# Performance work log

Hardware: AMD Instinct MI355X
Metric: run time of the kernel (lower is better)

Reference implementation:

```python
import jax, jax.numpy as jnp
import numpy as np

IMG_SIZE = 224
PATCH_SIZE = 16
CONTEXT_LEN = 316
LATENT_DIM = 1024
NUM_HEADS = 16
NUM_PATCHES = (IMG_SIZE // PATCH_SIZE) ** 2  # 196
SEQ_LEN = NUM_PATCHES + CONTEXT_LEN          # 512
BATCH = 8


def prefix_lm_mask(num_img_patches, total):
    # lower-triangular causal mask, but the image-patch block is fully bidirectional
    m = np.tril(np.ones((total, total), dtype=np.float32))
    m[:num_img_patches, :num_img_patches] = 1.0
    return jnp.asarray(m)  # [S, S], 1 = attend, 0 = masked


def setup_inputs() -> dict:
    key = jax.random.key(0)
    k_x, k_q, k_k, k_v, k_o, k_b = jax.random.split(key, 6)
    d = LATENT_DIM
    scale = 1.0 / np.sqrt(d)
    return {
        "x": jax.random.normal(k_x, (BATCH, SEQ_LEN, d), dtype=jnp.float32),
        "w_q": jax.random.normal(k_q, (d, d), dtype=jnp.float32) * scale,
        "w_k": jax.random.normal(k_k, (d, d), dtype=jnp.float32) * scale,
        "w_v": jax.random.normal(k_v, (d, d), dtype=jnp.float32) * scale,
        "w_o": jax.random.normal(k_o, (d, d), dtype=jnp.float32) * scale,
        "b_o": jax.random.normal(k_b, (d,), dtype=jnp.float32) * 0.01,
    }


def reference(x, w_q, w_k, w_v, w_o, b_o):
    B, S, D = x.shape
    H = NUM_HEADS
    hd = D // H
    # projections (nn.Linear: y = x @ W^T)
    q = (x @ w_q.T).reshape(B, S, H, hd).transpose(0, 2, 1, 3)  # [B,H,S,hd]
    k = (x @ w_k.T).reshape(B, S, H, hd).transpose(0, 2, 1, 3)
    v = (x @ w_v.T).reshape(B, S, H, hd).transpose(0, 2, 1, 3)
    scores = jnp.einsum("bhqd,bhkd->bhqk", q, k) / jnp.sqrt(jnp.float32(hd))
    mask = prefix_lm_mask(NUM_PATCHES, S)  # [S,S]
    scores = jnp.where(mask == 0, jnp.float32(-jnp.inf), scores)
    attn = jax.nn.softmax(scores, axis=-1)
    ctx = jnp.einsum("bhqk,bhkd->bhqd", attn, v)
    ctx = ctx.transpose(0, 2, 1, 3).reshape(B, S, D)
    return ctx @ w_o.T + b_o
```

## Files before the change

### kernel.cpp

```cpp
#include <hip/hip_runtime.h>
#include <stdint.h>
#include <math.h>

#define NB_B 8
#define NB_S 512
#define NB_D 1024
#define NB_H 16
#define NB_HD 64
#define NP 196
#define MTOT 4096

#define OFF_XB 0
#define OFF_WQ 4194304
#define OFF_WK 5242880
#define OFF_WV 6291456
#define OFF_WO 7340032
#define OFF_Q  8388608
#define OFF_K  12582912
#define OFF_VT 16777216
#define OFF_CT 20971520

typedef __attribute__((ext_vector_type(8))) short bf16x8;
typedef __attribute__((ext_vector_type(4))) float f32x4;
typedef __attribute__((ext_vector_type(4))) short s16x4;

__device__ __forceinline__ short f2bf(float f) {
  union { float f; uint32_t u; } c; c.f = f;
  uint32_t r = (c.u + 0x7fffu + ((c.u >> 16) & 1u)) >> 16;
  return (short)r;
}

__device__ __forceinline__ uint32_t pack2bf(float lo, float hi) {
  uint32_t ulo = __float_as_uint(lo) + 0x8000u;
  uint32_t uhi = __float_as_uint(hi) + 0x8000u;
  return __builtin_amdgcn_perm(uhi, ulo, 0x07060302u);
}

__device__ __forceinline__ void async16(void* lds, const void* g) {
  __builtin_amdgcn_global_load_lds(
      (const __attribute__((address_space(1))) void*)g,
      (__attribute__((address_space(3))) void*)lds, 16, 0, 0);
}

__global__ __launch_bounds__(256) void cvt5(const float* __restrict__ x,
                                            const float* __restrict__ wq,
                                            const float* __restrict__ wk,
                                            const float* __restrict__ wv,
                                            const float* __restrict__ wo,
                                            short* __restrict__ ws) {
  int b = blockIdx.x, t = threadIdx.x;
  const float* src; short* dst; float scale;
  if (b < 4096) { src = x + b * 1024; dst = ws + OFF_XB + b * 1024; scale = 1.0f; }
  else {
    int wb = b - 4096, wi = wb >> 10, r = wb & 1023;
    switch (wi) {
      case 0:  src = wq + r * 1024; dst = ws + OFF_WQ + r * 1024; scale = 0.125f; break;
      case 1:  src = wk + r * 1024; dst = ws + OFF_WK + r * 1024; scale = 1.0f;   break;
      case 2:  src = wv + r * 1024; dst = ws + OFF_WV + r * 1024; scale = 1.0f;   break;
      default: src = wo + r * 1024; dst = ws + OFF_WO + r * 1024; scale = 1.0f;   break;
    }
  }
  int i = t << 2;
  float4 v = *(const float4*)(src + i);
  s16x4 o;
  o[0] = f2bf(v.x * scale); o[1] = f2bf(v.y * scale);
  o[2] = f2bf(v.z * scale); o[3] = f2bf(v.w * scale);
  *(s16x4*)(dst + i) = o;
}

__global__ __launch_bounds__(256, 2) void gemm_qkv(short* __restrict__ ws) {
  __shared__ __align__(16) short As[4096];
  __shared__ __align__(16) short Bs[4096];
  int bx = blockIdx.x;
  int wsel = bx >> 8;
  int tile = bx & 255;
  int mt = tile >> 3, nt = tile & 7;
  int m0 = mt << 7, n0 = nt << 7;
  const short* A  = ws + OFF_XB;
  const short* Bw = ws + (wsel == 0 ? OFF_WQ : (wsel == 1 ? OFF_WK : OFF_WV));
  int t = threadIdx.x, lane = t & 63, wvi = t >> 6;
  int c = lane & 15, quad = lane >> 4;
  int wm = wvi >> 1, wn = wvi & 1;
  f32x4 acc[4][4] = {};

  for (int kk = 0; kk < 1024; kk += 32) {
#pragma unroll
    for (int i = 0; i < 2; ++i) {
      int ch = wvi * 2 + i;
      const short* ga = A  + (m0 + ch * 16 + c) * 1024 + kk + (quad << 3);
      async16(&As[ch << 9], ga);
      const short* gb = Bw + (n0 + ch * 16 + c) * 1024 + kk + (quad << 3);
      async16(&Bs[ch << 9], gb);
    }
    __syncthreads();
    bf16x8 af[4], bfr[4];
#pragma unroll
    for (int i = 0; i < 4; ++i) af[i]  = *(const bf16x8*)&As[((wm * 4 + i) * 64 + lane) * 8];
#pragma unroll
    for (int j = 0; j < 4; ++j) bfr[j] = *(const bf16x8*)&Bs[((wn * 4 + j) * 64 + lane) * 8];
#pragma unroll
    for (int i = 0; i < 4; ++i)
#pragma unroll
      for (int j = 0; j < 4; ++j)
        acc[i][j] = __builtin_amdgcn_mfma_f32_16x16x32_bf16(af[i], bfr[j], acc[i][j], 0, 0, 0);
    __syncthreads();
  }

  short* outp = ws + (wsel == 0 ? OFF_Q : (wsel == 1 ? OFF_K : OFF_VT));
#pragma unroll
  for (int i = 0; i < 4; ++i) {
#pragma unroll
    for (int j = 0; j < 4; ++j) {
      int n = n0 + wn * 64 + j * 16 + c;
      int h = n >> 6, d = n & 63;
      int mq = m0 + wm * 64 + i * 16 + quad * 4;
      int bb = mq >> 9, s = mq & 511;
      if (wsel < 2) {
#pragma unroll
        for (int r = 0; r < 4; ++r)
          outp[((bb * 16 + h) * 512 + (s + r)) * 64 + d] = f2bf(acc[i][j][r]);
      } else {
        s16x4 o;
#pragma unroll
        for (int r = 0; r < 4; ++r) o[r] = f2bf(acc[i][j][r]);
        *(s16x4*)&outp[((bb * 16 + h) * 64 + d) * 512 + s] = o;
      }
    }
  }
}

__global__ __launch_bounds__(256, 2) void attn(short* __restrict__ ws) {
  __shared__ __align__(16) short Kb[4096];
  __shared__ __align__(16) short Vb[4096];
  int bi = blockIdx.x;
  int bh = bi >> 2, qcr = bi & 3;
  int qc = (qcr + bh + 2 * (bh >> 6)) & 3;
  int t = threadIdx.x, lane = t & 63, wvi = t >> 6;
  int c = lane & 15, quad = lane >> 4;
  const short* Qh  = ws + OFF_Q  + bh * (512 * 64);
  const short* Kh  = ws + OFF_K  + bh * (512 * 64);
  const short* Vth = ws + OFF_VT + bh * (64 * 512);
  short* ctx = ws + OFF_CT;
  int b = bh >> 4, h = bh & 15;

  int qt0 = qc * 128 + wvi * 32;
  int qt1 = qt0 + 16;
  int kn0 = (qt0 + 16 > NP) ? (qt0 + 16) : NP;
  int kn1 = (qt1 + 16 > NP) ? (qt1 + 16) : NP;
  int knb = (qc * 128 + 128 > NP) ? (qc * 128 + 128) : NP;
  int NCH = (knb + 63) >> 6;

  bf16x8 q00 = *(const bf16x8*)(Qh + (qt0 + c) * 64 + (quad << 3));
  bf16x8 q01 = *(const bf16x8*)(Qh + (qt0 + c) * 64 + 32 + (quad << 3));
  bf16x8 q10 = *(const bf16x8*)(Qh + (qt1 + c) * 64 + (quad << 3));
  bf16x8 q11 = *(const bf16x8*)(Qh + (qt1 + c) * 64 + 32 + (quad << 3));

  f32x4 acc0[4] = {}, acc1[4] = {};
  float l0 = 0.0f, l1 = 0.0f;
  int L0 = c + ((quad & 1) << 5);
  bool hilo = quad >= 2;

  for (int ch = 0; ch < NCH; ++ch) {
    int k0 = ch << 6;
    {
      const short* gk = Kh + (k0 + wvi * 16 + c) * 64 + (quad << 3);
      async16(&Kb[(wvi * 2 + 0) << 9], gk);
      async16(&Kb[(wvi * 2 + 1) << 9], gk + 32);
      const short* gv = Vth + (wvi * 16 + c) * 512 + k0 + (quad << 3);
      async16(&Vb[(wvi * 2 + 0) << 9], gv);
      async16(&Vb[(wvi * 2 + 1) << 9], gv + 32);
    }
    __syncthreads();

    bf16x8 ak[4][2], av[4][2];
#pragma unroll
    for (int mb = 0; mb < 4; ++mb)
#pragma unroll
      for (int f = 0; f < 2; ++f) {
        ak[mb][f] = *(const bf16x8*)&Kb[((mb * 2 + f) << 9) + lane * 8];
        av[mb][f] = *(const bf16x8*)&Vb[((mb * 2 + f) << 9) + lane * 8];
      }

#pragma unroll
    for (int s = 0; s < 2; ++s) {
      int qt = s ? qt1 : qt0;
      int kn = s ? kn1 : kn0;
      if (k0 >= kn) continue;
      bf16x8 bq0 = s ? q10 : q00;
      bf16x8 bq1 = s ? q11 : q01;
      f32x4* acc = s ? acc1 : acc0;

      float p[4][4];
#pragma unroll
      for (int mb = 0; mb < 4; ++mb) {
        f32x4 st = {};
        st = __builtin_amdgcn_mfma_f32_16x16x32_bf16(ak[mb][0], bq0, st, 0, 0, 0);
        st = __builtin_amdgcn_mfma_f32_16x16x32_bf16(ak[mb][1], bq1, st, 0, 0, 0);
#pragma unroll
        for (int r = 0; r < 4; ++r) p[mb][r] = __expf(st[r]);
      }

      if ((k0 + 64 > NP) && (k0 + 64 > qt + 1)) {
        int row = qt + c;
#pragma unroll
        for (int mb = 0; mb < 4; ++mb)
#pragma unroll
          for (int r = 0; r < 4; ++r) {
            int key = k0 + mb * 16 + (quad << 2) + r;
            bool v = (row < NP) ? (key < NP) : (key <= row);
            p[mb][r] = v ? p[mb][r] : 0.0f;
          }
      }
      float ls = 0.0f;
#pragma unroll
      for (int mb = 0; mb < 4; ++mb)
#pragma unroll
        for (int r = 0; r < 4; ++r) ls += p[mb][r];
      if (s) l1 += ls; else l0 += ls;

#pragma unroll
      for (int hh = 0; hh < 2; ++hh) {
        float* pa = p[2 * hh];
        float* pb = p[2 * hh + 1];
        uint32_t e0 = pack2bf(pa[0], pa[1]);
        uint32_t e1 = pack2bf(pa[2], pa[3]);
        uint32_t e2 = pack2bf(pb[0], pb[1]);
        uint32_t e3 = pack2bf(pb[2], pb[3]);
        uint32_t a0 = (uint32_t)__shfl((int)e0, L0);
        uint32_t b0 = (uint32_t)__shfl((int)e1, L0);
        uint32_t a1 = (uint32_t)__shfl((int)e0, L0 + 16);
        uint32_t b1 = (uint32_t)__shfl((int)e1, L0 + 16);
        uint32_t c0 = (uint32_t)__shfl((int)e2, L0);
        uint32_t d0 = (uint32_t)__shfl((int)e3, L0);
        uint32_t c1 = (uint32_t)__shfl((int)e2, L0 + 16);
        uint32_t d1 = (uint32_t)__shfl((int)e3, L0 + 16);
        union { uint32_t u[4]; bf16x8 v; } bp;
        bp.u[0] = hilo ? c0 : a0;
        bp.u[1] = hilo ? d0 : b0;
        bp.u[2] = hilo ? c1 : a1;
        bp.u[3] = hilo ? d1 : b1;
#pragma unroll
        for (int db = 0; db < 4; ++db)
          acc[db] = __builtin_amdgcn_mfma_f32_16x16x32_bf16(av[db][hh], bp.v, acc[db], 0, 0, 0);
      }
    }
    __syncthreads();
  }

#pragma unroll
  for (int s = 0; s < 2; ++s) {
    float l = s ? l1 : l0;
    f32x4* acc = s ? acc1 : acc0;
    int qt = s ? qt1 : qt0;
    l += __shfl_xor(l, 16);
    l += __shfl_xor(l, 32);
    float inv = 1.0f / l;
    size_t rowbase = ((size_t)(b * 512 + qt + c)) * 1024 + h * 64 + (quad << 2);
#pragma unroll
    for (int db = 0; db < 4; ++db) {
      s16x4 o;
#pragma unroll
      for (int r = 0; r < 4; ++r) o[r] = f2bf(acc[db][r] * inv);
      *(s16x4*)&ctx[rowbase + db * 16] = o;
    }
  }
}

__global__ __launch_bounds__(256, 2) void gemm_out(const short* __restrict__ ws,
                                                   const float* __restrict__ bias,
                                                   float* __restrict__ out) {
  __shared__ __align__(16) short As[4096];
  __shared__ __align__(16) short Bs[4096];
  int tile = blockIdx.x;
  int mt = tile >> 3, nt = tile & 7;
  int m0 = mt << 7, n0 = nt << 7;
  const short* A  = ws + OFF_CT;
  const short* Bw = ws + OFF_WO;
  int t = threadIdx.x, lane = t & 63, wvi = t >> 6;
  int c = lane & 15, quad = lane >> 4;
  int wm = wvi >> 1, wn = wvi & 1;
  f32x4 acc[4][4] = {};

  for (int kk = 0; kk < 1024; kk += 32) {
#pragma unroll
    for (int i = 0; i < 2; ++i) {
      int ch = wvi * 2 + i;
      async16(&As[ch << 9], A  + (m0 + ch * 16 + c) * 1024 + kk + (quad << 3));
      async16(&Bs[ch << 9], Bw + (n0 + ch * 16 + c) * 1024 + kk + (quad << 3));
    }
    __syncthreads();
    bf16x8 af[4], bfr[4];
#pragma unroll
    for (int i = 0; i < 4; ++i) af[i]  = *(const bf16x8*)&As[((wm * 4 + i) * 64 + lane) * 8];
#pragma unroll
    for (int j = 0; j < 4; ++j) bfr[j] = *(const bf16x8*)&Bs[((wn * 4 + j) * 64 + lane) * 8];
#pragma unroll
    for (int i = 0; i < 4; ++i)
#pragma unroll
      for (int j = 0; j < 4; ++j)
        acc[i][j] = __builtin_amdgcn_mfma_f32_16x16x32_bf16(af[i], bfr[j], acc[i][j], 0, 0, 0);
    __syncthreads();
  }

#pragma unroll
  for (int j = 0; j < 4; ++j) {
    int n = n0 + wn * 64 + j * 16 + c;
    float bj = bias[n];
#pragma unroll
    for (int i = 0; i < 4; ++i) {
      int mq = m0 + wm * 64 + i * 16 + quad * 4;
#pragma unroll
      for (int r = 0; r < 4; ++r)
        out[(size_t)(mq + r) * 1024 + n] = acc[i][j][r] + bj;
    }
  }
}

extern "C" void kernel_launch(void* const* d_in, const int* in_sizes, int n_in,
                              void* d_out, int out_size, void* d_ws, size_t ws_size,
                              hipStream_t stream) {
  (void)in_sizes; (void)n_in; (void)out_size; (void)ws_size;
  const float* x  = (const float*)d_in[0];
  const float* wq = (const float*)d_in[1];
  const float* wk = (const float*)d_in[2];
  const float* wv = (const float*)d_in[3];
  const float* wo = (const float*)d_in[4];
  const float* bo = (const float*)d_in[5];
  short* ws = (short*)d_ws;
  float* out = (float*)d_out;

  cvt5<<<8192, 256, 0, stream>>>(x, wq, wk, wv, wo, ws);
  gemm_qkv<<<768, 256, 0, stream>>>(ws);
  attn<<<512, 256, 0, stream>>>(ws);
  gemm_out<<<256, 256, 0, stream>>>(ws, bo, out);
}
```

Before: 188.6 us.

## Fuse Q, K, V projections into one GEMM tile sharing the activation tile

The QKV projection kernel now gives each block a 64-row slice of x and computes 128 columns of all three of Q, K and V together. Each loaded A tile is reused across the three weight matrices instead of being reloaded by three separate blocks. This cuts global and LDS traffic for the activations and shrinks the grid from 768 to 512 blocks. In exchange, LDS use rises to about 28 KB per block and each wave holds 24 accumulator tiles, which raises register pressure and may lower occupancy.

Result: slower. 195.1 us (+3.4%).

```diff
diff --git a/kernel.cpp b/kernel.cpp
--- a/kernel.cpp
+++ b/kernel.cpp
@@ -69,61 +69,67 @@
 }
 
 __global__ __launch_bounds__(256, 2) void gemm_qkv(short* __restrict__ ws) {
-  __shared__ __align__(16) short As[4096];
-  __shared__ __align__(16) short Bs[4096];
+  __shared__ __align__(16) short Ls[14336];
   int bx = blockIdx.x;
-  int wsel = bx >> 8;
-  int tile = bx & 255;
-  int mt = tile >> 3, nt = tile & 7;
-  int m0 = mt << 7, n0 = nt << 7;
-  const short* A  = ws + OFF_XB;
-  const short* Bw = ws + (wsel == 0 ? OFF_WQ : (wsel == 1 ? OFF_WK : OFF_WV));
+  int mt = bx >> 3, nt = bx & 7;
+  int m0 = mt << 6, n0 = nt << 7;
+  const short* A = ws + OFF_XB;
   int t = threadIdx.x, lane = t & 63, wvi = t >> 6;
   int c = lane & 15, quad = lane >> 4;
-  int wm = wvi >> 1, wn = wvi & 1;
-  f32x4 acc[4][4] = {};
+  f32x4 acc[3][4][2] = {};
 
   for (int kk = 0; kk < 1024; kk += 32) {
 #pragma unroll
-    for (int i = 0; i < 2; ++i) {
-      int ch = wvi * 2 + i;
-      const short* ga = A  + (m0 + ch * 16 + c) * 1024 + kk + (quad << 3);
-      async16(&As[ch << 9], ga);
-      const short* gb = Bw + (n0 + ch * 16 + c) * 1024 + kk + (quad << 3);
-      async16(&Bs[ch << 9], gb);
-    }
-    __syncthreads();
-    bf16x8 af[4], bfr[4];
-#pragma unroll
-    for (int i = 0; i < 4; ++i) af[i]  = *(const bf16x8*)&As[((wm * 4 + i) * 64 + lane) * 8];
-#pragma unroll
-    for (int j = 0; j < 4; ++j) bfr[j] = *(const bf16x8*)&Bs[((wn * 4 + j) * 64 + lane) * 8];
-#pragma unroll
-    for (int i = 0; i < 4; ++i)
-#pragma unroll
-      for (int j = 0; j < 4; ++j)
-        acc[i][j] = __builtin_amdgcn_mfma_f32_16x16x32_bf16(af[i], bfr[j], acc[i][j], 0, 0, 0);
-    __syncthreads();
-  }
-
-  short* outp = ws + (wsel == 0 ? OFF_Q : (wsel == 1 ? OFF_K : OFF_VT));
-#pragma unroll
-  for (int i = 0; i < 4; ++i) {
-#pragma unroll
-    for (int j = 0; j < 4; ++j) {
-      int n = n0 + wn * 64 + j * 16 + c;
+    for (int i = 0; i < 7; ++i) {
+      int ch = wvi * 7 + i;
+      const short* src;
+      if (ch < 4) {
+        src = A + (m0 + ch * 16 + c) * 1024 + kk + (quad << 3);
+      } else {
+        int cw = (ch - 4) >> 3, cb = (ch - 4) & 7;
+        src = ws + OFF_WQ + cw * 1048576 + (n0 + cb * 16 + c) * 1024 + kk + (quad << 3);
+      }
+      async16(&Ls[ch << 9], src);
+    }
+    __syncthreads();
+
+    bf16x8 af[4];
+#pragma unroll
+    for (int mb = 0; mb < 4; ++mb) af[mb] = *(const bf16x8*)&Ls[(mb << 9) + lane * 8];
+#pragma unroll
+    for (int w = 0; w < 3; ++w) {
+#pragma unroll
+      for (int nb = 0; nb < 2; ++nb) {
+        bf16x8 bf = *(const bf16x8*)&Ls[((4 + w * 8 + wvi * 2 + nb) << 9) + lane * 8];
+#pragma unroll
+        for (int mb = 0; mb < 4; ++mb)
+          acc[w][mb][nb] = __builtin_amdgcn_mfma_f32_16x16x32_bf16(af[mb], bf, acc[w][mb][nb], 0, 0, 0);
+      }
+    }
+    __syncthreads();
+  }
+
+#pragma unroll
+  for (int w = 0; w < 3; ++w) {
+#pragma unroll
+    for (int nb = 0; nb < 2; ++nb) {
+      int n = n0 + wvi * 32 + nb * 16 + c;
       int h = n >> 6, d = n & 63;
-      int mq = m0 + wm * 64 + i * 16 + quad * 4;
-      int bb = mq >> 9, s = mq & 511;
-      if (wsel < 2) {
-#pragma unroll
-        for (int r = 0; r < 4; ++r)
-          outp[((bb * 16 + h) * 512 + (s + r)) * 64 + d] = f2bf(acc[i][j][r]);
-      } else {
-        s16x4 o;
-#pragma unroll
-        for (int r = 0; r < 4; ++r) o[r] = f2bf(acc[i][j][r]);
-        *(s16x4*)&outp[((bb * 16 + h) * 64 + d) * 512 + s] = o;
+#pragma unroll
+      for (int mb = 0; mb < 4; ++mb) {
+        int m = m0 + mb * 16 + (quad << 2);
+        int bb = m >> 9, s = m & 511;
+        if (w < 2) {
+          short* outp = ws + OFF_Q + w * 4194304;
+#pragma unroll
+          for (int r = 0; r < 4; ++r)
+            outp[((bb * 16 + h) * 512 + s + r) * 64 + d] = f2bf(acc[w][mb][nb][r]);
+        } else {
+          s16x4 o;
+#pragma unroll
+          for (int r = 0; r < 4; ++r) o[r] = f2bf(acc[w][mb][nb][r]);
+          *(s16x4*)&ws[OFF_VT + ((bb * 16 + h) * 64 + d) * 512 + s] = o;
+        }
       }
     }
   }
@@ -330,7 +336,7 @@
   float* out = (float*)d_out;
 
   cvt5<<<8192, 256, 0, stream>>>(x, wq, wk, wv, wo, ws);
-  gemm_qkv<<<768, 256, 0, stream>>>(ws);
+  gemm_qkv<<<512, 256, 0, stream>>>(ws);
   attn<<<512, 256, 0, stream>>>(ws);
   gemm_out<<<256, 256, 0, stream>>>(ws, bo, out);
 }
```
